# Kernel optimization log

Measured on AMD Instinct MI355X. Metric: run time of the kernel, lower is better.

## Reference

```python
import jax, jax.numpy as jnp
import numpy as np

INDIM = 256
NUM_CENTERS = 1024
OUTDIM = 128
N = 65536


def setup_inputs() -> dict:
    key = jax.random.key(0)
    kx, kc, kw, kb = jax.random.split(key, 4)
    x = jax.random.normal(kx, (N, INDIM), dtype=jnp.float32)
    # centers ~ U(-1, 1), sigmas = 0.1 as in init_centers_sigmas
    centers = jax.random.uniform(kc, (NUM_CENTERS, INDIM), dtype=jnp.float32, minval=-1.0, maxval=1.0)
    sigmas = jnp.full((NUM_CENTERS,), 0.1, dtype=jnp.float32)
    # nn.Linear(num_centers, outdim): weight [outdim, num_centers], bias [outdim]
    bound = 1.0 / np.sqrt(NUM_CENTERS)
    W = jax.random.uniform(kw, (OUTDIM, NUM_CENTERS), dtype=jnp.float32, minval=-bound, maxval=bound)
    b = jax.random.uniform(kb, (OUTDIM,), dtype=jnp.float32, minval=-bound, maxval=bound)
    return {"x": x, "centers": centers, "sigmas": sigmas, "W": W, "b": b}


def reference(x, centers, sigmas, W, b):
    # phi[n, m] = exp(-sigma_m * ||x_n - c_m||^2)
    x_sq = jnp.sum(x * x, axis=1)               # [N]
    c_sq = jnp.sum(centers * centers, axis=1)   # [M]
    cross = jnp.einsum('nd,md->nm', x, centers) # [N, M]
    sqdist = x_sq[:, None] + c_sq[None, :] - 2.0 * cross
    phi = jnp.exp(-sigmas[None, :] * sqdist)    # [N, M]
    return phi @ W.T + b                        # [N, outdim]
```

## Files before the change

### kernel.cpp

```cpp
#include <hip/hip_runtime.h>

typedef __attribute__((ext_vector_type(8))) short bf16x8;
typedef __attribute__((ext_vector_type(4))) float f32x4;
typedef __attribute__((ext_vector_type(2))) long long2v;
typedef unsigned int u32;
typedef unsigned long long u64;

#define LOG2E 1.44269504088896f

__device__ __forceinline__ short f2bf(float f) {
    union { float f; unsigned u; } v; v.f = f;
    unsigned r = v.u + 0x7fffu + ((v.u >> 16) & 1u);
    return (short)(r >> 16);
}

__device__ __forceinline__ u32 f2e4m3(float f) {
    u32 u = __float_as_uint(f);
    u32 sgn = (u >> 24) & 0x80u;
    u32 mag = u & 0x7fffffffu;
    if (mag >= 0x43E00000u) return sgn | 0x7Eu;
    if (mag < 0x3C800000u) {
        u32 q = (u32)(__uint_as_float(mag) * 512.0f + 0.5f);
        return sgn | q;
    }
    u32 r = mag + 0x0007FFFFu + ((mag >> 20) & 1u);
    u32 e8 = ((r >> 23) - 120u) & 0xFu;
    u32 m3 = (r >> 20) & 7u;
    return sgn | (e8 << 3) | m3;
}

__device__ __forceinline__ long pack8_e4m3(float4 a, float4 b) {
    u32 lo = f2e4m3(a.x) | (f2e4m3(a.y) << 8) | (f2e4m3(a.z) << 16) | (f2e4m3(a.w) << 24);
    u32 hi = f2e4m3(b.x) | (f2e4m3(b.y) << 8) | (f2e4m3(b.z) << 16) | (f2e4m3(b.w) << 24);
    return (long)(((u64)hi << 32) | lo);
}

#if __has_builtin(__builtin_amdgcn_exp2f)
#define EXP2(x) __builtin_amdgcn_exp2f(x)
#else
#define EXP2(x) __builtin_exp2f(x)
#endif

__device__ __forceinline__ u32 pack_bf16_trunc(float lo, float hi) {
#if __has_builtin(__builtin_amdgcn_perm)
    return __builtin_amdgcn_perm(__float_as_uint(hi), __float_as_uint(lo), 0x07060302u);
#else
    return (__float_as_uint(hi) & 0xFFFF0000u) | (__float_as_uint(lo) >> 16);
#endif
}

__device__ __forceinline__ void gload16(const void* g, void* l) {
    __builtin_amdgcn_global_load_lds(
        (const __attribute__((address_space(1))) void*)g,
        (__attribute__((address_space(3))) void*)l, 16, 0, 0);
}

__global__ __launch_bounds__(256) void rbf_prep(
    const float* __restrict__ centers, const float* __restrict__ sigmas,
    const float* __restrict__ W,
    char* __restrict__ cfrag8, short* __restrict__ wfrag,
    float* __restrict__ nscsp, float* __restrict__ tsp)
{
    const int tid = threadIdx.x;
    const int bid = blockIdx.x;
    if (bid < 256) {
        const int lane = tid & 63, w = tid >> 6;
        const int m = bid * 4 + w;
        const float4 v = ((const float4*)(centers + (size_t)m * 256))[lane];
        float s = v.x*v.x + v.y*v.y + v.z*v.z + v.w*v.w;
        #pragma unroll
        for (int off = 32; off >= 1; off >>= 1) s += __shfl_xor(s, off, 64);
        if (lane == 0) {
            const float sg = sigmas[m];
            const int c = m >> 5, w5 = m & 31;
            const int g = w5 >> 3, r = w5 & 7, h = r >> 2, j = r & 3;
            const int slot = ((c * 2 + h) * 4 + g) * 4 + j;
            nscsp[slot] = -sg * s * LOG2E;
            tsp[slot]   = 2.0f * sg * LOG2E;
        }
    } else if (bid < 320) {
        const int s = (bid - 256) * 256 + tid;
        const int c = s >> 9, ks = (s >> 6) & 7, lane = s & 63;
        const int l15 = lane & 15;
        const int k = ks * 32 + (lane >> 4) * 8;
        long2v t;
        #pragma unroll
        for (int h = 0; h < 2; ++h) {
            const int m = c * 32 + 8 * (l15 >> 2) + 4 * h + (l15 & 3);
            const float4 a = *(const float4*)(centers + (size_t)m * 256 + k);
            const float4 b = *(const float4*)(centers + (size_t)m * 256 + k + 4);
            t[h] = pack8_e4m3(a, b);
        }
        *(long2v*)(cfrag8 + (size_t)s * 16) = t;
    } else {
        const int s = (bid - 320) * 256 + tid;
        const int c = s >> 9, ot = (s >> 6) & 7, lane = s & 63;
        const int o = ot * 16 + (lane & 15);
        const int k = c * 32 + (lane >> 4) * 8;
        const float4 a = *(const float4*)(W + (size_t)o * 1024 + k);
        const float4 b = *(const float4*)(W + (size_t)o * 1024 + k + 4);
        bf16x8 t;
        t[0]=f2bf(a.x); t[1]=f2bf(a.y); t[2]=f2bf(a.z); t[3]=f2bf(a.w);
        t[4]=f2bf(b.x); t[5]=f2bf(b.y); t[6]=f2bf(b.z); t[7]=f2bf(b.w);
        ((bf16x8*)wfrag)[s] = t;
    }
}

__global__ __launch_bounds__(256, 2) void rbf_main(
    const float* __restrict__ x, const float* __restrict__ bvec,
    const char* __restrict__ cfrag8, const short* __restrict__ wfrag,
    const float* __restrict__ nscsp, const float* __restrict__ tsp,
    float* __restrict__ out)
{
    __shared__ char   Cb8[4][8192];
    __shared__ float4 Tls[512];

    const int tid = threadIdx.x;
    const int lane = tid & 63;
    const int l15 = lane & 15;
    const int g4 = lane >> 4;
    const int w = tid >> 6;
    const int qb = blockIdx.x * 128 + w * 32;

#define STAGEC(ci, slot) do {                                                      \
        const char* _cs = cfrag8 + (size_t)(ci) * 8192 + w * 2048 + lane * 16;     \
        gload16(_cs,        &Cb8[(slot)][w * 2048]);                               \
        gload16(_cs + 1024, &Cb8[(slot)][w * 2048 + 1024]);                        \
    } while (0)

#define SEXP(slot, cc, pa0, pa1) do {                                              \
        f32x4 s00 = (f32x4){0.f,0.f,0.f,0.f}, s01 = s00, s10 = s00, s11 = s00;     \
        const char* cb = &Cb8[(slot)][0] + (size_t)lane * 16;                      \
        _Pragma("unroll")                                                          \
        for (int ks = 0; ks < 8; ++ks) {                                           \
            const long2v A = *(const long2v*)(cb + ks * 1024);                     \
            s00 = __builtin_amdgcn_mfma_f32_16x16x32_fp8_fp8(A[0], xq8[0][ks], s00, 0, 0, 0); \
            s10 = __builtin_amdgcn_mfma_f32_16x16x32_fp8_fp8(A[0], xq8[1][ks], s10, 0, 0, 0); \
            s01 = __builtin_amdgcn_mfma_f32_16x16x32_fp8_fp8(A[1], xq8[0][ks], s01, 0, 0, 0); \
            s11 = __builtin_amdgcn_mfma_f32_16x16x32_fp8_fp8(A[1], xq8[1][ks], s11, 0, 0, 0); \
        }                                                                          \
        const int base0 = ((cc) * 2 + 0) * 4 + g4;                                 \
        const int base1 = ((cc) * 2 + 1) * 4 + g4;                                 \
        const float4 q0 = Tls[base0];                                              \
        const float4 t0 = Tls[256 + base0];                                        \
        const float4 q1 = Tls[base1];                                              \
        const float4 t1 = Tls[256 + base1];                                        \
        const float* q0p = (const float*)&q0; const float* t0p = (const float*)&t0;\
        const float* q1p = (const float*)&q1; const float* t1p = (const float*)&t1;\
        float p00[4], p01[4], p10[4], p11[4];                                      \
        _Pragma("unroll")                                                          \
        for (int j = 0; j < 4; ++j) {                                              \
            p00[j] = EXP2(fmaf(t0p[j], s00[j] - hxs0, q0p[j]));                    \
            p01[j] = EXP2(fmaf(t1p[j], s01[j] - hxs0, q1p[j]));                    \
            p10[j] = EXP2(fmaf(t0p[j], s10[j] - hxs1, q0p[j]));                    \
            p11[j] = EXP2(fmaf(t1p[j], s11[j] - hxs1, q1p[j]));                    \
        }                                                                          \
        pa0.u[0] = pack_bf16_trunc(p00[0], p00[1]);                                \
        pa0.u[1] = pack_bf16_trunc(p00[2], p00[3]);                                \
        pa0.u[2] = pack_bf16_trunc(p01[0], p01[1]);                                \
        pa0.u[3] = pack_bf16_trunc(p01[2], p01[3]);                                \
        pa1.u[0] = pack_bf16_trunc(p10[0], p10[1]);                                \
        pa1.u[1] = pack_bf16_trunc(p10[2], p10[3]);                                \
        pa1.u[2] = pack_bf16_trunc(p11[0], p11[1]);                                \
        pa1.u[3] = pack_bf16_trunc(p11[2], p11[3]);                                \
    } while (0)

#define PV(pa0, pa1, wv) do {                                                      \
        _Pragma("unroll")                                                          \
        for (int ot = 0; ot < 8; ++ot) {                                           \
            acc[0][ot] = __builtin_amdgcn_mfma_f32_16x16x32_bf16(pa0.v, wv[ot], acc[0][ot], 0, 0, 0); \
            acc[1][ot] = __builtin_amdgcn_mfma_f32_16x16x32_bf16(pa1.v, wv[ot], acc[1][ot], 0, 0, 0); \
        }                                                                          \
    } while (0)

    STAGEC(0, 0);
    STAGEC(1, 1);

    Tls[tid]       = ((const float4*)nscsp)[tid];
    Tls[256 + tid] = ((const float4*)tsp)[tid];

    long xq8[2][8];
    float xs[2];
    #pragma unroll
    for (int t = 0; t < 2; ++t) {
        const float* xr = x + (size_t)(qb + t * 16 + l15) * 256 + g4 * 8;
        float ss = 0.f;
        #pragma unroll
        for (int ks = 0; ks < 8; ++ks) {
            const float4 a = *(const float4*)(xr + ks * 32);
            const float4 b = *(const float4*)(xr + ks * 32 + 4);
            ss += a.x*a.x + a.y*a.y + a.z*a.z + a.w*a.w
                + b.x*b.x + b.y*b.y + b.z*b.z + b.w*b.w;
            xq8[t][ks] = pack8_e4m3(a, b);
        }
        ss += __shfl_xor(ss, 16, 64);
        ss += __shfl_xor(ss, 32, 64);
        xs[t] = ss;
    }
    const float hxs0 = 0.5f * xs[0];
    const float hxs1 = 0.5f * xs[1];

    f32x4 acc[2][8];
    #pragma unroll
    for (int t = 0; t < 2; ++t)
        #pragma unroll
        for (int ot = 0; ot < 8; ++ot) acc[t][ot] = (f32x4){0.f, 0.f, 0.f, 0.f};

    __syncthreads();

    const bf16x8* wsrc = (const bf16x8*)wfrag + lane;

    for (int i = 0; i < 16; ++i) {
        const int cA = 2 * i, cB = 2 * i + 1;
        const int sA = (i & 1) * 2, sB = sA + 1;

        bf16x8 wA[8];
        #pragma unroll
        for (int f = 0; f < 8; ++f) wA[f] = wsrc[(size_t)cA * 512 + f * 64];

        if (i < 15) {
            STAGEC(cA + 2, sA ^ 2);
            STAGEC(cB + 2, sB ^ 2);
        }

        union { u32 u[4]; bf16x8 v; } paA0, paA1, paB0, paB1;
        SEXP(sA, cA, paA0, paA1);

        bf16x8 wB[8];
        #pragma unroll
        for (int f = 0; f < 8; ++f) wB[f] = wsrc[(size_t)cB * 512 + f * 64];

        PV(paA0, paA1, wA);
        SEXP(sB, cB, paB0, paB1);
        PV(paB0, paB1, wB);

        if (i < 15) __syncthreads();
    }

    #pragma unroll
    for (int t = 0; t < 2; ++t) {
        #pragma unroll
        for (int jr = 0; jr < 4; ++jr) {
            const int q = qb + t * 16 + g4 * 4 + jr;
            #pragma unroll
            for (int ot = 0; ot < 8; ++ot)
                out[(size_t)q * 128 + ot * 16 + l15] = acc[t][ot][jr] + bvec[ot * 16 + l15];
        }
    }
#undef STAGEC
#undef SEXP
#undef PV
}

extern "C" void kernel_launch(void* const* d_in, const int* in_sizes, int n_in,
                              void* d_out, int out_size, void* d_ws, size_t ws_size,
                              hipStream_t stream) {
    (void)in_sizes; (void)n_in; (void)out_size; (void)ws_size;
    const float* x       = (const float*)d_in[0];
    const float* centers = (const float*)d_in[1];
    const float* sigmas  = (const float*)d_in[2];
    const float* W       = (const float*)d_in[3];
    const float* b       = (const float*)d_in[4];
    float* out = (float*)d_out;

    char*  cfrag8 = (char*)d_ws;
    short* wfrag  = (short*)(cfrag8 + 16384 * 16);
    float* nscsp  = (float*)(wfrag + 16384 * 8);
    float* tsp    = nscsp + 1024;

    rbf_prep<<<384, 256, 0, stream>>>(centers, sigmas, W, cfrag8, wfrag, nscsp, tsp);
    rbf_main<<<512, 256, 0, stream>>>(x, b, cfrag8, wfrag, nscsp, tsp, out);
}
```

Measured before the change: 70.06 us.

## Shrink blocks to two waves with triple-buffered center staging and MFMA priority

Blocks drop from 4 waves to 2 waves (64 rows each), and the grid doubles to 1024. Each wave now stages half of an 8KB center chunk. The two-chunk double-buffered loop becomes a per-chunk loop over a 3-slot ring with a partial vmcnt wait and a raw s_barrier, which lets the next-next chunk load while the current one is computed. s_setprio is raised around the MFMA sections to favor matrix issue across waves. Smaller blocks and less shared memory could allow more resident blocks, but each block still reloads all centers and W, so global and L2 traffic per output row rises.

```diff
diff --git a/kernel.cpp b/kernel.cpp
--- a/kernel.cpp
+++ b/kernel.cpp
@@ -106,13 +106,13 @@
     }
 }
 
-__global__ __launch_bounds__(256, 2) void rbf_main(
+__global__ __launch_bounds__(128, 2) void rbf_main(
     const float* __restrict__ x, const float* __restrict__ bvec,
     const char* __restrict__ cfrag8, const short* __restrict__ wfrag,
     const float* __restrict__ nscsp, const float* __restrict__ tsp,
     float* __restrict__ out)
 {
-    __shared__ char   Cb8[4][8192];
+    __shared__ char   Cb8[3][8192];
     __shared__ float4 Tls[512];
 
     const int tid = threadIdx.x;
@@ -120,17 +120,20 @@
     const int l15 = lane & 15;
     const int g4 = lane >> 4;
     const int w = tid >> 6;
-    const int qb = blockIdx.x * 128 + w * 32;
-
-#define STAGEC(ci, slot) do {                                                      \
-        const char* _cs = cfrag8 + (size_t)(ci) * 8192 + w * 2048 + lane * 16;     \
-        gload16(_cs,        &Cb8[(slot)][w * 2048]);                               \
-        gload16(_cs + 1024, &Cb8[(slot)][w * 2048 + 1024]);                        \
+    const int qb = blockIdx.x * 64 + w * 32;
+
+#define STAGE(ci, slot) do {                                                       \
+        const char* _cs = cfrag8 + (size_t)(ci) * 8192 + w * 4096 + lane * 16;     \
+        gload16(_cs,        &Cb8[(slot)][w * 4096]);                               \
+        gload16(_cs + 1024, &Cb8[(slot)][w * 4096 + 1024]);                        \
+        gload16(_cs + 2048, &Cb8[(slot)][w * 4096 + 2048]);                        \
+        gload16(_cs + 3072, &Cb8[(slot)][w * 4096 + 3072]);                        \
     } while (0)
 
 #define SEXP(slot, cc, pa0, pa1) do {                                              \
         f32x4 s00 = (f32x4){0.f,0.f,0.f,0.f}, s01 = s00, s10 = s00, s11 = s00;     \
         const char* cb = &Cb8[(slot)][0] + (size_t)lane * 16;                      \
+        __builtin_amdgcn_s_setprio(1);                                             \
         _Pragma("unroll")                                                          \
         for (int ks = 0; ks < 8; ++ks) {                                           \
             const long2v A = *(const long2v*)(cb + ks * 1024);                     \
@@ -139,6 +142,7 @@
             s01 = __builtin_amdgcn_mfma_f32_16x16x32_fp8_fp8(A[1], xq8[0][ks], s01, 0, 0, 0); \
             s11 = __builtin_amdgcn_mfma_f32_16x16x32_fp8_fp8(A[1], xq8[1][ks], s11, 0, 0, 0); \
         }                                                                          \
+        __builtin_amdgcn_s_setprio(0);                                             \
         const int base0 = ((cc) * 2 + 0) * 4 + g4;                                 \
         const int base1 = ((cc) * 2 + 1) * 4 + g4;                                 \
         const float4 q0 = Tls[base0];                                              \
@@ -166,18 +170,22 @@
     } while (0)
 
 #define PV(pa0, pa1, wv) do {                                                      \
+        __builtin_amdgcn_s_setprio(1);                                             \
         _Pragma("unroll")                                                          \
         for (int ot = 0; ot < 8; ++ot) {                                           \
             acc[0][ot] = __builtin_amdgcn_mfma_f32_16x16x32_bf16(pa0.v, wv[ot], acc[0][ot], 0, 0, 0); \
             acc[1][ot] = __builtin_amdgcn_mfma_f32_16x16x32_bf16(pa1.v, wv[ot], acc[1][ot], 0, 0, 0); \
         }                                                                          \
+        __builtin_amdgcn_s_setprio(0);                                             \
     } while (0)
 
-    STAGEC(0, 0);
-    STAGEC(1, 1);
+    STAGE(0, 0);
+    STAGE(1, 1);
 
     Tls[tid]       = ((const float4*)nscsp)[tid];
+    Tls[128 + tid] = ((const float4*)nscsp)[128 + tid];
     Tls[256 + tid] = ((const float4*)tsp)[tid];
+    Tls[384 + tid] = ((const float4*)tsp)[128 + tid];
 
     long xq8[2][8];
     float xs[2];
@@ -210,31 +218,23 @@
 
     const bf16x8* wsrc = (const bf16x8*)wfrag + lane;
 
-    for (int i = 0; i < 16; ++i) {
-        const int cA = 2 * i, cB = 2 * i + 1;
-        const int sA = (i & 1) * 2, sB = sA + 1;
-
-        bf16x8 wA[8];
-        #pragma unroll
-        for (int f = 0; f < 8; ++f) wA[f] = wsrc[(size_t)cA * 512 + f * 64];
-
-        if (i < 15) {
-            STAGEC(cA + 2, sA ^ 2);
-            STAGEC(cB + 2, sB ^ 2);
-        }
-
-        union { u32 u[4]; bf16x8 v; } paA0, paA1, paB0, paB1;
-        SEXP(sA, cA, paA0, paA1);
-
-        bf16x8 wB[8];
-        #pragma unroll
-        for (int f = 0; f < 8; ++f) wB[f] = wsrc[(size_t)cB * 512 + f * 64];
-
-        PV(paA0, paA1, wA);
-        SEXP(sB, cB, paB0, paB1);
-        PV(paB0, paB1, wB);
-
-        if (i < 15) __syncthreads();
+    for (int c = 0; c < 32; ++c) {
+        const int slot = c % 3;
+
+        bf16x8 wv[8];
+        #pragma unroll
+        for (int f = 0; f < 8; ++f) wv[f] = wsrc[(size_t)c * 512 + f * 64];
+
+        if (c < 30) STAGE(c + 2, (c + 2) % 3);
+
+        union { u32 u[4]; bf16x8 v; } pa0, pa1;
+        SEXP(slot, c, pa0, pa1);
+        PV(pa0, pa1, wv);
+
+        if (c < 31) {
+            asm volatile("s_waitcnt vmcnt(4)" ::: "memory");
+            __builtin_amdgcn_s_barrier();
+        }
     }
 
     #pragma unroll
@@ -247,7 +247,7 @@
                 out[(size_t)q * 128 + ot * 16 + l15] = acc[t][ot][jr] + bvec[ot * 16 + l15];
         }
     }
-#undef STAGEC
+#undef STAGE
 #undef SEXP
 #undef PV
 }
@@ -269,5 +269,5 @@
     float* tsp    = nscsp + 1024;
 
     rbf_prep<<<384, 256, 0, stream>>>(centers, sigmas, W, cfrag8, wfrag, nscsp, tsp);
-    rbf_main<<<512, 256, 0, stream>>>(x, b, cfrag8, wfrag, nscsp, tsp, out);
-}
+    rbf_main<<<1024, 128, 0, stream>>>(x, b, cfrag8, wfrag, nscsp, tsp, out);
+}
```

After: 74.31 us. 1.06x slower.

## Deepen center staging to four slots and prefetch LDS fragments into registers

Applied to the files above, without the earlier changes.

Restructures the main loop into per-chunk steps with a 4-slot LDS ring staged three chunks ahead. The next chunk's center fragments are read from LDS into registers (double-buffered rX/rY) before the current chunk's MFMAs run. The full __syncthreads is replaced by a manual vmcnt wait plus s_barrier on every chunk. The aim is to hide global-load and LDS latency behind MFMA work, at the cost of more registers and one barrier per chunk instead of one per pair.

```diff
diff --git a/kernel.cpp b/kernel.cpp
--- a/kernel.cpp
+++ b/kernel.cpp
@@ -122,22 +122,26 @@
     const int w = tid >> 6;
     const int qb = blockIdx.x * 128 + w * 32;
 
-#define STAGEC(ci, slot) do {                                                      \
+#define STAGE(ci, slot) do {                                                       \
         const char* _cs = cfrag8 + (size_t)(ci) * 8192 + w * 2048 + lane * 16;     \
         gload16(_cs,        &Cb8[(slot)][w * 2048]);                               \
         gload16(_cs + 1024, &Cb8[(slot)][w * 2048 + 1024]);                        \
     } while (0)
 
-#define SEXP(slot, cc, pa0, pa1) do {                                              \
+#define PREF(ci, rv) do {                                                          \
+        const char* _cb = &Cb8[(ci) & 3][0] + (size_t)lane * 16;                   \
+        _Pragma("unroll")                                                          \
+        for (int ks = 0; ks < 8; ++ks) rv[ks] = *(const long2v*)(_cb + ks * 1024); \
+    } while (0)
+
+#define SEXPR(rv, cc, pa0, pa1) do {                                               \
         f32x4 s00 = (f32x4){0.f,0.f,0.f,0.f}, s01 = s00, s10 = s00, s11 = s00;     \
-        const char* cb = &Cb8[(slot)][0] + (size_t)lane * 16;                      \
         _Pragma("unroll")                                                          \
         for (int ks = 0; ks < 8; ++ks) {                                           \
-            const long2v A = *(const long2v*)(cb + ks * 1024);                     \
-            s00 = __builtin_amdgcn_mfma_f32_16x16x32_fp8_fp8(A[0], xq8[0][ks], s00, 0, 0, 0); \
-            s10 = __builtin_amdgcn_mfma_f32_16x16x32_fp8_fp8(A[0], xq8[1][ks], s10, 0, 0, 0); \
-            s01 = __builtin_amdgcn_mfma_f32_16x16x32_fp8_fp8(A[1], xq8[0][ks], s01, 0, 0, 0); \
-            s11 = __builtin_amdgcn_mfma_f32_16x16x32_fp8_fp8(A[1], xq8[1][ks], s11, 0, 0, 0); \
+            s00 = __builtin_amdgcn_mfma_f32_16x16x32_fp8_fp8(rv[ks][0], xq8[0][ks], s00, 0, 0, 0); \
+            s10 = __builtin_amdgcn_mfma_f32_16x16x32_fp8_fp8(rv[ks][0], xq8[1][ks], s10, 0, 0, 0); \
+            s01 = __builtin_amdgcn_mfma_f32_16x16x32_fp8_fp8(rv[ks][1], xq8[0][ks], s01, 0, 0, 0); \
+            s11 = __builtin_amdgcn_mfma_f32_16x16x32_fp8_fp8(rv[ks][1], xq8[1][ks], s11, 0, 0, 0); \
         }                                                                          \
         const int base0 = ((cc) * 2 + 0) * 4 + g4;                                 \
         const int base1 = ((cc) * 2 + 1) * 4 + g4;                                 \
@@ -165,7 +169,7 @@
         pa1.u[3] = pack_bf16_trunc(p11[2], p11[3]);                                \
     } while (0)
 
-#define PV(pa0, pa1, wv) do {                                                      \
+#define PVX(pa0, pa1, wv) do {                                                     \
         _Pragma("unroll")                                                          \
         for (int ot = 0; ot < 8; ++ot) {                                           \
             acc[0][ot] = __builtin_amdgcn_mfma_f32_16x16x32_bf16(pa0.v, wv[ot], acc[0][ot], 0, 0, 0); \
@@ -173,8 +177,25 @@
         }                                                                          \
     } while (0)
 
-    STAGEC(0, 0);
-    STAGEC(1, 1);
+#define CHUNK(c, cur, nxt) do {                                                    \
+        bf16x8 wv[8];                                                              \
+        _Pragma("unroll")                                                          \
+        for (int f = 0; f < 8; ++f) wv[f] = wsrc[(size_t)(c) * 512 + f * 64];      \
+        if ((c) <= 28) STAGE((c) + 3, ((c) + 3) & 3);                              \
+        if ((c) <= 30) PREF((c) + 1, nxt);                                         \
+        union { u32 u[4]; bf16x8 v; } pa0, pa1;                                    \
+        SEXPR(cur, (c), pa0, pa1);                                                 \
+        PVX(pa0, pa1, wv);                                                         \
+        if ((c) < 31) {                                                            \
+            if ((c) <= 28) { asm volatile("s_waitcnt vmcnt(2)" ::: "memory"); }    \
+            else           { asm volatile("s_waitcnt vmcnt(0)" ::: "memory"); }    \
+            __builtin_amdgcn_s_barrier();                                          \
+        }                                                                          \
+    } while (0)
+
+    STAGE(0, 0);
+    STAGE(1, 1);
+    STAGE(2, 2);
 
     Tls[tid]       = ((const float4*)nscsp)[tid];
     Tls[256 + tid] = ((const float4*)tsp)[tid];
@@ -210,31 +231,13 @@
 
     const bf16x8* wsrc = (const bf16x8*)wfrag + lane;
 
+    long2v rX[8], rY[8];
+    PREF(0, rX);
+
+    #pragma unroll 2
     for (int i = 0; i < 16; ++i) {
-        const int cA = 2 * i, cB = 2 * i + 1;
-        const int sA = (i & 1) * 2, sB = sA + 1;
-
-        bf16x8 wA[8];
-        #pragma unroll
-        for (int f = 0; f < 8; ++f) wA[f] = wsrc[(size_t)cA * 512 + f * 64];
-
-        if (i < 15) {
-            STAGEC(cA + 2, sA ^ 2);
-            STAGEC(cB + 2, sB ^ 2);
-        }
-
-        union { u32 u[4]; bf16x8 v; } paA0, paA1, paB0, paB1;
-        SEXP(sA, cA, paA0, paA1);
-
-        bf16x8 wB[8];
-        #pragma unroll
-        for (int f = 0; f < 8; ++f) wB[f] = wsrc[(size_t)cB * 512 + f * 64];
-
-        PV(paA0, paA1, wA);
-        SEXP(sB, cB, paB0, paB1);
-        PV(paB0, paB1, wB);
-
-        if (i < 15) __syncthreads();
+        CHUNK(2 * i,     rX, rY);
+        CHUNK(2 * i + 1, rY, rX);
     }
 
     #pragma unroll
@@ -247,9 +250,11 @@
                 out[(size_t)q * 128 + ot * 16 + l15] = acc[t][ot][jr] + bvec[ot * 16 + l15];
         }
     }
-#undef STAGEC
-#undef SEXP
-#undef PV
+#undef STAGE
+#undef PREF
+#undef SEXPR
+#undef PVX
+#undef CHUNK
 }
 
 extern "C" void kernel_launch(void* const* d_in, const int* in_sizes, int n_in,
```

Result: no change. 70.51 us (+0.6%).
